# Optimization experiments

Hardware: AMD Instinct MI355X
Metric: run time of the kernel (lower is better)

## Reference

```python
import jax, jax.numpy as jnp
import numpy as np
from jax import lax

BLOCK_LEN = 128  # ctx_len 8192 / blocks 64
NEG_INF = -1e9


def setup_inputs() -> dict:
    key = jax.random.key(0)
    ks = jax.random.split(key, 8)
    N, L, Dm = 2, 8192, 4096
    W, H, dh = 1024, 16, 64  # width = d_model*0.25
    s = lambda fan: 1.0 / np.sqrt(fan)
    return {
        "inputs": jax.random.normal(ks[0], (N, L, Dm), jnp.float32),
        "conv_w": jax.random.normal(ks[1], (3, Dm, 3 * W), jnp.float32) * s(3 * Dm),
        "conv_b": jnp.zeros((3 * W,), jnp.float32),
        "wq": jax.random.normal(ks[2], (W, H, dh), jnp.float32) * s(W),
        "bq": jnp.zeros((H, dh), jnp.float32),
        "wk": jax.random.normal(ks[3], (W, H, dh), jnp.float32) * s(W),
        "bk": jnp.zeros((H, dh), jnp.float32),
        "wv": jax.random.normal(ks[4], (W, H, dh), jnp.float32) * s(W),
        "bv": jnp.zeros((H, dh), jnp.float32),
        "wo": jax.random.normal(ks[5], (H, dh, W), jnp.float32) * s(H * dh),
        "bo": jnp.zeros((W,), jnp.float32),
        "proj_w": jax.random.normal(ks[6], (W, Dm), jnp.float32) * s(W),
        "proj_b": jnp.zeros((Dm,), jnp.float32),
    }


def reference(inputs, conv_w, conv_b, wq, bq, wk, bk, wv, bv, wo, bo, proj_w, proj_b):
    N, L, Dm = inputs.shape
    # Conv1D(kernel=3, same padding) producing q,k,v concatenated
    x = lax.conv_general_dilated(
        inputs, conv_w, window_strides=(1,), padding="SAME",
        dimension_numbers=("NWC", "WIO", "NWC")) + conv_b
    q, k, v = jnp.split(x, 3, axis=-1)  # each [N, L, W]
    W_ = q.shape[-1]
    nb = L // BLOCK_LEN
    # row attention: independent causal attention within each block
    q = q.reshape(N * nb, BLOCK_LEN, W_)
    k = k.reshape(N * nb, BLOCK_LEN, W_)
    v = v.reshape(N * nb, BLOCK_LEN, W_)
    dh = wq.shape[-1]
    qh = jnp.einsum("btd,dhe->bthe", q, wq) + bq  # [B, T, H, dh]
    kh = jnp.einsum("btd,dhe->bthe", k, wk) + bk
    vh = jnp.einsum("btd,dhe->bthe", v, wv) + bv
    scale = 1.0 / jnp.sqrt(jnp.asarray(dh, qh.dtype))
    scores = jnp.einsum("bqhe,bkhe->bhqk", qh * scale, kh)
    causal = jnp.tril(jnp.ones((BLOCK_LEN, BLOCK_LEN), bool))
    scores = jnp.where(causal, scores, NEG_INF)
    p = jax.nn.softmax(scores, axis=-1)
    o = jnp.einsum("bhqk,bkhe->bqhe", p, vh)
    o = jnp.einsum("bqhe,hed->bqd", o, wo) + bo  # MHA output projection -> width
    o = o.reshape(N, L, W_)
    return o @ proj_w + proj_b  # final Dense(d_model)
```

## Files before the change

kernel.cpp:

```cpp
#include <hip/hip_runtime.h>
#include <hip/hip_bf16.h>
#include <stdint.h>

typedef __attribute__((ext_vector_type(8))) short short8;
typedef __attribute__((ext_vector_type(4))) float f32x4;

#define AS1 __attribute__((address_space(1)))
#define AS3 __attribute__((address_space(3)))

__device__ __forceinline__ short f2bf(float x) {
    __hip_bfloat16 h = __float2bfloat16(x);
    union { __hip_bfloat16 h; short s; } u; u.h = h; return u.s;
}

__device__ __forceinline__ void gload_lds16(const short* g, short* l) {
    __builtin_amdgcn_global_load_lds((const AS1 void*)g, (AS3 void*)l, 16, 0, 0);
}

#define BAR()        asm volatile("s_barrier" ::: "memory")
#define VMCNT_BAR(N) asm volatile("s_waitcnt vmcnt(" #N ")\n\ts_barrier" ::: "memory")

template<int TAPS, bool F32OUT>
__global__ __launch_bounds__(512, 2) void gemm256(
    const short* __restrict__ A, int lda,
    const short* __restrict__ BT, int ldb, long long tapB,
    void* __restrict__ Cout, int ldc,
    const float* __restrict__ bias, int Ktiles)
{
    __shared__ __align__(16) short As[2 * 2 * 256 * 32];
    __shared__ __align__(16) short Bs[2 * 2 * 256 * 32];
    const int tid = threadIdx.x, lane = tid & 63, wid = tid >> 6;
    const int wm = wid >> 2, wn = wid & 3;
    const int m0 = blockIdx.y * 256, n0 = blockIdx.x * 256;
    const size_t arow0 = (TAPS == 3) ? ((size_t)(m0 >> 13) * 8194 + (size_t)(m0 & 8191))
                                     : (size_t)m0;
    const size_t ldaS = (size_t)lda, ldbS = (size_t)ldb, tapBS = (size_t)tapB;
    const short* Abase0 = A + arow0 * ldaS;
    const short* Bbase0 = BT + (size_t)n0 * ldbS;
    const int c15 = lane & 15, g4 = (lane >> 4) * 4;
    const int swz = ((lane >> 4) ^ ((c15 >> 1) & 3)) * 8;
    const int srow = tid >> 2;
    const int schunk = (((tid & 3) ^ ((tid >> 3) & 3)) * 8);

#define STG_A(u, kh, buf) do { \
    const int tp_ = (TAPS == 3) ? ((u) >> 6) : 0; \
    const int kc_ = (TAPS == 3) ? (((u) & 63) << 6) : ((u) << 6); \
    const short* g_ = Abase0 + (size_t)tp_ * ldaS + kc_ + (kh) * 32 \
                      + (size_t)srow * ldaS + schunk; \
    short* l_ = As + (buf) * 16384 + (kh) * 8192 + wid * 512; \
    gload_lds16(g_, l_); \
    gload_lds16(g_ + 128 * ldaS, l_ + 4096); \
} while (0)

#define STG_B(u, kh, buf) do { \
    const int tp_ = (TAPS == 3) ? ((u) >> 6) : 0; \
    const int kc_ = (TAPS == 3) ? (((u) & 63) << 6) : ((u) << 6); \
    const short* g_ = Bbase0 + (size_t)tp_ * tapBS + kc_ + (kh) * 32 \
                      + (size_t)srow * ldbS + schunk; \
    short* l_ = Bs + (buf) * 16384 + (kh) * 8192 + wid * 512; \
    gload_lds16(g_, l_); \
    gload_lds16(g_ + 128 * ldbS, l_ + 4096); \
} while (0)

#define LDA_(buf, kk, mi) (*(const short8*)(As + (buf) * 16384 + (kk) * 8192 \
                           + (wm * 128 + (mi) * 16 + c15) * 32 + swz))
#define LDB_(buf, kk, nj) (*(const short8*)(Bs + (buf) * 16384 + (kk) * 8192 \
                           + (wn * 64 + (nj) * 16 + c15) * 32 + swz))

#define MFMA8x2(J0, J1) do { \
    __builtin_amdgcn_s_setprio(1); \
    _Pragma("unroll") \
    for (int mi_ = 0; mi_ < 8; ++mi_) \
        acc[mi_][J0] = __builtin_amdgcn_mfma_f32_16x16x32_bf16(af[mi_], b0, acc[mi_][J0], 0, 0, 0); \
    _Pragma("unroll") \
    for (int mi_ = 0; mi_ < 8; ++mi_) \
        acc[mi_][J1] = __builtin_amdgcn_mfma_f32_16x16x32_bf16(af[mi_], b1, acc[mi_][J1], 0, 0, 0); \
    __builtin_amdgcn_s_setprio(0); \
} while (0)

    f32x4 acc[8][4];
    #pragma unroll
    for (int i = 0; i < 8; ++i)
        #pragma unroll
        for (int j = 0; j < 4; ++j)
            acc[i][j] = (f32x4){0.f, 0.f, 0.f, 0.f};

    STG_A(0, 0, 0); STG_B(0, 0, 0); STG_A(0, 1, 0); STG_B(0, 1, 0);
    VMCNT_BAR(4);

    for (int t = 0; t < Ktiles; ++t) {
        const int c = t & 1, nb = c ^ 1;
        const bool st = (t + 1 < Ktiles);
        const int u = t + 1;
        short8 af[8], b0, b1;

        #pragma unroll
        for (int mi = 0; mi < 8; ++mi) af[mi] = LDA_(c, 0, mi);
        b0 = LDB_(c, 0, 0); b1 = LDB_(c, 0, 1);
        if (st) STG_A(u, 0, nb);
        BAR();
        MFMA8x2(0, 1);
        BAR();

        b0 = LDB_(c, 0, 2); b1 = LDB_(c, 0, 3);
        if (st) STG_B(u, 0, nb);
        if (st) { VMCNT_BAR(4); } else { VMCNT_BAR(0); }
        MFMA8x2(2, 3);
        BAR();

        #pragma unroll
        for (int mi = 0; mi < 8; ++mi) af[mi] = LDA_(c, 1, mi);
        b0 = LDB_(c, 1, 0); b1 = LDB_(c, 1, 1);
        if (st) STG_A(u, 1, nb);
        BAR();
        MFMA8x2(0, 1);
        BAR();

        b0 = LDB_(c, 1, 2); b1 = LDB_(c, 1, 3);
        if (st) STG_B(u, 1, nb);
        if (st) { VMCNT_BAR(4); } else { VMCNT_BAR(0); }
        MFMA8x2(2, 3);
        BAR();
    }

    float bv[4];
    #pragma unroll
    for (int nj = 0; nj < 4; ++nj)
        bv[nj] = bias ? bias[n0 + wn * 64 + nj * 16 + c15] : 0.f;
    #pragma unroll
    for (int mi = 0; mi < 8; ++mi) {
        #pragma unroll
        for (int r = 0; r < 4; ++r) {
            const size_t row = (size_t)m0 + wm * 128 + mi * 16 + g4 + r;
            #pragma unroll
            for (int nj = 0; nj < 4; ++nj) {
                const int col = n0 + wn * 64 + nj * 16 + c15;
                const float v = acc[mi][nj][r] + bv[nj];
                if (F32OUT) ((float*)Cout)[row * (size_t)ldc + col] = v;
                else        ((short*)Cout)[row * (size_t)ldc + col] = f2bf(v);
            }
        }
    }
#undef STG_A
#undef STG_B
#undef LDA_
#undef LDB_
#undef MFMA8x2
}

__global__ __launch_bounds__(256) void attn_kernel(
    const short* __restrict__ qh, const short* __restrict__ kh,
    const short* __restrict__ vh, short* __restrict__ obuf)
{
    __shared__ __align__(16) char smem[54272];
    short* qs = (short*)smem;
    short* ks = (short*)smem + 9216;
    short* vt = (short*)(smem + 36864);
    short* ps = (short*)smem;
    short* os = (short*)smem;

    const int tid = threadIdx.x, lane = tid & 63, wid = tid >> 6;
    const int h = blockIdx.x, b = blockIdx.y;
    const size_t base = (size_t)b * 128 * 1024 + (size_t)h * 64;

    for (int i = tid; i < 1024; i += 256) {
        const int row = i >> 3, c8 = i & 7;
        const size_t g = base + (size_t)row * 1024 + c8 * 8;
        *(short8*)(qs + row * 72 + c8 * 8) = *(const short8*)(qh + g);
        *(short8*)(ks + row * 72 + c8 * 8) = *(const short8*)(kh + g);
        short8 vv = *(const short8*)(vh + g);
        #pragma unroll
        for (int j = 0; j < 8; ++j) vt[(c8 * 8 + j) * 136 + row] = vv[j];
    }
    __syncthreads();

    const int c15 = lane & 15, g8 = (lane >> 4) * 8, g4 = (lane >> 4) * 4;
    const int r0 = wid * 32;

    f32x4 sacc[2][8];
    #pragma unroll
    for (int mi = 0; mi < 2; ++mi)
        #pragma unroll
        for (int nj = 0; nj < 8; ++nj)
            sacc[mi][nj] = (f32x4){0.f, 0.f, 0.f, 0.f};
    #pragma unroll
    for (int kk = 0; kk < 2; ++kk) {
        short8 aq[2];
        #pragma unroll
        for (int mi = 0; mi < 2; ++mi)
            aq[mi] = *(const short8*)(qs + (r0 + mi * 16 + c15) * 72 + kk * 32 + g8);
        #pragma unroll
        for (int nj = 0; nj < 8; ++nj) {
            short8 bk8 = *(const short8*)(ks + (nj * 16 + c15) * 72 + kk * 32 + g8);
            #pragma unroll
            for (int mi = 0; mi < 2; ++mi)
                sacc[mi][nj] = __builtin_amdgcn_mfma_f32_16x16x32_bf16(
                    aq[mi], bk8, sacc[mi][nj], 0, 0, 0);
        }
    }
    __syncthreads();

    #pragma unroll
    for (int mi = 0; mi < 2; ++mi) {
        #pragma unroll
        for (int r = 0; r < 4; ++r) {
            const int qrow = r0 + mi * 16 + g4 + r;
            float m = -3.0e38f, pv[8];
            #pragma unroll
            for (int nj = 0; nj < 8; ++nj) {
                float s = sacc[mi][nj][r] * 0.125f;
                if (nj * 16 + c15 > qrow) s = -1.0e9f;
                pv[nj] = s; m = fmaxf(m, s);
            }
            #pragma unroll
            for (int off = 8; off >= 1; off >>= 1) m = fmaxf(m, __shfl_xor(m, off));
            float sum = 0.f;
            #pragma unroll
            for (int nj = 0; nj < 8; ++nj) { float p = __expf(pv[nj] - m); pv[nj] = p; sum += p; }
            #pragma unroll
            for (int off = 8; off >= 1; off >>= 1) sum += __shfl_xor(sum, off);
            const float inv = 1.0f / sum;
            #pragma unroll
            for (int nj = 0; nj < 8; ++nj)
                ps[qrow * 136 + nj * 16 + c15] = f2bf(pv[nj] * inv);
        }
    }
    __syncthreads();

    f32x4 oacc[2][4];
    #pragma unroll
    for (int mi = 0; mi < 2; ++mi)
        #pragma unroll
        for (int nj = 0; nj < 4; ++nj)
            oacc[mi][nj] = (f32x4){0.f, 0.f, 0.f, 0.f};
    #pragma unroll
    for (int kt = 0; kt < 4; ++kt) {
        short8 ap[2];
        #pragma unroll
        for (int mi = 0; mi < 2; ++mi)
            ap[mi] = *(const short8*)(ps + (r0 + mi * 16 + c15) * 136 + kt * 32 + g8);
        #pragma unroll
        for (int nj = 0; nj < 4; ++nj) {
            short8 bv8 = *(const short8*)(vt + (nj * 16 + c15) * 136 + kt * 32 + g8);
            #pragma unroll
            for (int mi = 0; mi < 2; ++mi)
                oacc[mi][nj] = __builtin_amdgcn_mfma_f32_16x16x32_bf16(
                    ap[mi], bv8, oacc[mi][nj], 0, 0, 0);
        }
    }
    __syncthreads();

    #pragma unroll
    for (int mi = 0; mi < 2; ++mi)
        #pragma unroll
        for (int r = 0; r < 4; ++r)
            #pragma unroll
            for (int nj = 0; nj < 4; ++nj)
                os[(r0 + mi * 16 + g4 + r) * 72 + nj * 16 + c15] = f2bf(oacc[mi][nj][r]);
    __syncthreads();

    for (int i = tid; i < 1024; i += 256) {
        const int row = i >> 3, c8 = i & 7;
        *(short8*)(obuf + base + (size_t)row * 1024 + c8 * 8) =
            *(const short8*)(os + row * 72 + c8 * 8);
    }
}

__global__ void pad_convert_inputs(const float* __restrict__ in, short* __restrict__ out)
{
    const int row = blockIdx.x;
    const int n = row / 8194, l = row % 8194;
    short* orow = out + (size_t)row * 4096;
    if (l == 0 || l == 8193) {
        for (int i = threadIdx.x; i < 512; i += 256) {
            uint4 z; z.x = z.y = z.z = z.w = 0u;
            *(uint4*)(orow + i * 8) = z;
        }
    } else {
        const float* irow = in + ((size_t)n * 8192 + (l - 1)) * 4096;
        for (int i = threadIdx.x; i < 512; i += 256) {
            float4 a = *(const float4*)(irow + i * 8);
            float4 b = *(const float4*)(irow + i * 8 + 4);
            short8 v;
            v[0] = f2bf(a.x); v[1] = f2bf(a.y); v[2] = f2bf(a.z); v[3] = f2bf(a.w);
            v[4] = f2bf(b.x); v[5] = f2bf(b.y); v[6] = f2bf(b.z); v[7] = f2bf(b.w);
            *(short8*)(orow + i * 8) = v;
        }
    }
}

__global__ void transpose_convert(const float* __restrict__ in, short* __restrict__ out,
                                  int R, int C)
{
    __shared__ float tile[32][33];
    const int tx = threadIdx.x & 31, ty = threadIdx.x >> 5;
    const int bx = blockIdx.x * 32, by = blockIdx.y * 32;
    #pragma unroll
    for (int i = 0; i < 32; i += 8)
        tile[ty + i][tx] = in[(size_t)(by + ty + i) * C + bx + tx];
    __syncthreads();
    #pragma unroll
    for (int i = 0; i < 32; i += 8)
        out[(size_t)(bx + ty + i) * R + by + tx] = f2bf(tile[tx][ty + i]);
}

__global__ void convert_bf16(const float* __restrict__ in, short* __restrict__ out, int n8)
{
    const int idx = blockIdx.x * 256 + threadIdx.x;
    if (idx < n8) {
        float4 a = *(const float4*)(in + (size_t)idx * 8);
        float4 b = *(const float4*)(in + (size_t)idx * 8 + 4);
        short8 v;
        v[0] = f2bf(a.x); v[1] = f2bf(a.y); v[2] = f2bf(a.z); v[3] = f2bf(a.w);
        v[4] = f2bf(b.x); v[5] = f2bf(b.y); v[6] = f2bf(b.z); v[7] = f2bf(b.w);
        *(short8*)(out + (size_t)idx * 8) = v;
    }
}

__global__ void fuse_bias(const float* __restrict__ bo, const float* __restrict__ projw,
                          const float* __restrict__ projb, float* __restrict__ outb)
{
    const int j = blockIdx.x * 256 + threadIdx.x;
    float s = projb[j];
    for (int w = 0; w < 1024; ++w) s = fmaf(bo[w], projw[(size_t)w * 4096 + j], s);
    outb[j] = s;
}

extern "C" void kernel_launch(void* const* d_in, const int* in_sizes, int n_in,
                              void* d_out, int out_size, void* d_ws, size_t ws_size,
                              hipStream_t stream)
{
    const float* inputs = (const float*)d_in[0];
    const float* conv_w = (const float*)d_in[1];
    const float* conv_b = (const float*)d_in[2];
    const float* wq     = (const float*)d_in[3];
    const float* bq     = (const float*)d_in[4];
    const float* wk     = (const float*)d_in[5];
    const float* bk     = (const float*)d_in[6];
    const float* wv     = (const float*)d_in[7];
    const float* bv     = (const float*)d_in[8];
    const float* wo     = (const float*)d_in[9];
    const float* bo     = (const float*)d_in[10];
    const float* proj_w = (const float*)d_in[11];
    const float* proj_b = (const float*)d_in[12];

    char* ws = (char*)d_ws;
    short* in_pad = (short*)(ws + 0);
    short* w_bf   = (short*)(ws + 134283264);
    short* qkv    = (short*)(ws + 209780736);
    short* wq_t   = (short*)(ws + 310444032);
    short* wk_t   = (short*)(ws + 312541184);
    short* wv_t   = (short*)(ws + 314638336);
    short* wo_bf  = (short*)(ws + 316735488);
    short* proj_t = (short*)(ws + 318832640);
    short* WfT    = (short*)(ws + 327221248);
    float* bfused = (float*)(ws + 335609856);
    short* qh_buf = (short*)(ws + 0);
    short* kh_buf = (short*)(ws + 33554432);
    short* vh_buf = (short*)(ws + 67108864);
    short* o_buf  = (short*)(ws + 134283264);

    dim3 blk(256), blk5(512);

    pad_convert_inputs<<<16388, blk, 0, stream>>>(inputs, in_pad);
    for (int t = 0; t < 3; ++t)
        transpose_convert<<<dim3(96, 128), blk, 0, stream>>>(
            conv_w + (size_t)t * 4096 * 3072, w_bf + (size_t)t * 3072 * 4096, 4096, 3072);
    transpose_convert<<<dim3(32, 32), blk, 0, stream>>>(wq, wq_t, 1024, 1024);
    transpose_convert<<<dim3(32, 32), blk, 0, stream>>>(wk, wk_t, 1024, 1024);
    transpose_convert<<<dim3(32, 32), blk, 0, stream>>>(wv, wv_t, 1024, 1024);
    transpose_convert<<<dim3(128, 32), blk, 0, stream>>>(proj_w, proj_t, 1024, 4096);
    convert_bf16<<<512, blk, 0, stream>>>(wo, wo_bf, 131072);
    fuse_bias<<<16, blk, 0, stream>>>(bo, proj_w, proj_b, bfused);

    gemm256<1, false><<<dim3(4, 16), blk5, 0, stream>>>(
        proj_t, 1024, wo_bf, 1024, 0, WfT, 1024, nullptr, 16);
    gemm256<3, false><<<dim3(12, 64), blk5, 0, stream>>>(
        in_pad, 4096, w_bf, 4096, (long long)3072 * 4096, qkv, 3072, conv_b, 192);
    gemm256<1, false><<<dim3(4, 64), blk5, 0, stream>>>(
        qkv + 0,    3072, wq_t, 1024, 0, qh_buf, 1024, bq, 16);
    gemm256<1, false><<<dim3(4, 64), blk5, 0, stream>>>(
        qkv + 1024, 3072, wk_t, 1024, 0, kh_buf, 1024, bk, 16);
    gemm256<1, false><<<dim3(4, 64), blk5, 0, stream>>>(
        qkv + 2048, 3072, wv_t, 1024, 0, vh_buf, 1024, bv, 16);

    attn_kernel<<<dim3(16, 128), blk, 0, stream>>>(qh_buf, kh_buf, vh_buf, o_buf);

    gemm256<1, true><<<dim3(16, 64), blk5, 0, stream>>>(
        o_buf, 1024, WfT, 1024, 0, d_out, 4096, bfused, 16);
}
```

Before: 1.729 ms.

## Double-buffer GEMM LDS fragments in registers and prefetch across MFMA blocks

Restructures the gemm256 main loop so A/B fragments for the next MFMA block are loaded from LDS while the current 4x4 block of MFMAs runs. Fragments of the next tile are prefetched before the loop back. The MFMAs are regrouped into 4x4 sub-tiles and several barriers are dropped, with one lgkmcnt wait plus barrier at the end of each iteration. The aim is to hide LDS read latency behind matrix work and cut synchronisation, at the cost of more live vector registers and a possible spill risk under the 512x2 launch bound.

```diff
diff --git a/kernel.cpp b/kernel.cpp
--- a/kernel.cpp
+++ b/kernel.cpp
@@ -19,6 +19,7 @@
 
 #define BAR()        asm volatile("s_barrier" ::: "memory")
 #define VMCNT_BAR(N) asm volatile("s_waitcnt vmcnt(" #N ")\n\ts_barrier" ::: "memory")
+#define LGKM0_BAR()  asm volatile("s_waitcnt lgkmcnt(0)\n\ts_barrier" ::: "memory")
 
 template<int TAPS, bool F32OUT>
 __global__ __launch_bounds__(512, 2) void gemm256(
@@ -67,14 +68,15 @@
 #define LDB_(buf, kk, nj) (*(const short8*)(Bs + (buf) * 16384 + (kk) * 8192 \
                            + (wn * 64 + (nj) * 16 + c15) * 32 + swz))
 
-#define MFMA8x2(J0, J1) do { \
+#define MM(mi, nj, Av, Bv) acc[mi][nj] = \
+    __builtin_amdgcn_mfma_f32_16x16x32_bf16(Av, Bv, acc[mi][nj], 0, 0, 0)
+
+#define MFMA16(MB, A0, A1, A2, A3, B0, B1, B2, B3) do { \
     __builtin_amdgcn_s_setprio(1); \
-    _Pragma("unroll") \
-    for (int mi_ = 0; mi_ < 8; ++mi_) \
-        acc[mi_][J0] = __builtin_amdgcn_mfma_f32_16x16x32_bf16(af[mi_], b0, acc[mi_][J0], 0, 0, 0); \
-    _Pragma("unroll") \
-    for (int mi_ = 0; mi_ < 8; ++mi_) \
-        acc[mi_][J1] = __builtin_amdgcn_mfma_f32_16x16x32_bf16(af[mi_], b1, acc[mi_][J1], 0, 0, 0); \
+    MM((MB)+0, 0, A0, B0); MM((MB)+0, 1, A0, B1); MM((MB)+0, 2, A0, B2); MM((MB)+0, 3, A0, B3); \
+    MM((MB)+1, 0, A1, B0); MM((MB)+1, 1, A1, B1); MM((MB)+1, 2, A1, B2); MM((MB)+1, 3, A1, B3); \
+    MM((MB)+2, 0, A2, B0); MM((MB)+2, 1, A2, B1); MM((MB)+2, 2, A2, B2); MM((MB)+2, 3, A2, B3); \
+    MM((MB)+3, 0, A3, B0); MM((MB)+3, 1, A3, B1); MM((MB)+3, 2, A3, B2); MM((MB)+3, 3, A3, B3); \
     __builtin_amdgcn_s_setprio(0); \
 } while (0)
 
@@ -85,42 +87,47 @@
         for (int j = 0; j < 4; ++j)
             acc[i][j] = (f32x4){0.f, 0.f, 0.f, 0.f};
 
+    short8 afC0, afC1, afC2, afC3;
+    short8 afN0, afN1, afN2, afN3;
+    short8 bC0, bC1, bC2, bC3;
+    short8 bN0, bN1, bN2, bN3;
+
     STG_A(0, 0, 0); STG_B(0, 0, 0); STG_A(0, 1, 0); STG_B(0, 1, 0);
     VMCNT_BAR(4);
+    afC0 = LDA_(0, 0, 0); afC1 = LDA_(0, 0, 1); afC2 = LDA_(0, 0, 2); afC3 = LDA_(0, 0, 3);
+    bC0 = LDB_(0, 0, 0); bC1 = LDB_(0, 0, 1); bC2 = LDB_(0, 0, 2); bC3 = LDB_(0, 0, 3);
 
     for (int t = 0; t < Ktiles; ++t) {
         const int c = t & 1, nb = c ^ 1;
         const bool st = (t + 1 < Ktiles);
         const int u = t + 1;
-        short8 af[8], b0, b1;
-
-        #pragma unroll
-        for (int mi = 0; mi < 8; ++mi) af[mi] = LDA_(c, 0, mi);
-        b0 = LDB_(c, 0, 0); b1 = LDB_(c, 0, 1);
+
         if (st) STG_A(u, 0, nb);
         BAR();
-        MFMA8x2(0, 1);
-        BAR();
-
-        b0 = LDB_(c, 0, 2); b1 = LDB_(c, 0, 3);
+        afN0 = LDA_(c, 0, 4); afN1 = LDA_(c, 0, 5); afN2 = LDA_(c, 0, 6); afN3 = LDA_(c, 0, 7);
+        MFMA16(0, afC0, afC1, afC2, afC3, bC0, bC1, bC2, bC3);
+
         if (st) STG_B(u, 0, nb);
         if (st) { VMCNT_BAR(4); } else { VMCNT_BAR(0); }
-        MFMA8x2(2, 3);
-        BAR();
-
-        #pragma unroll
-        for (int mi = 0; mi < 8; ++mi) af[mi] = LDA_(c, 1, mi);
-        b0 = LDB_(c, 1, 0); b1 = LDB_(c, 1, 1);
+        afC0 = LDA_(c, 1, 0); afC1 = LDA_(c, 1, 1); afC2 = LDA_(c, 1, 2); afC3 = LDA_(c, 1, 3);
+        bN0 = LDB_(c, 1, 0); bN1 = LDB_(c, 1, 1); bN2 = LDB_(c, 1, 2); bN3 = LDB_(c, 1, 3);
+        MFMA16(4, afN0, afN1, afN2, afN3, bC0, bC1, bC2, bC3);
+
         if (st) STG_A(u, 1, nb);
         BAR();
-        MFMA8x2(0, 1);
-        BAR();
-
-        b0 = LDB_(c, 1, 2); b1 = LDB_(c, 1, 3);
+        afN0 = LDA_(c, 1, 4); afN1 = LDA_(c, 1, 5); afN2 = LDA_(c, 1, 6); afN3 = LDA_(c, 1, 7);
+        MFMA16(0, afC0, afC1, afC2, afC3, bN0, bN1, bN2, bN3);
+
         if (st) STG_B(u, 1, nb);
         if (st) { VMCNT_BAR(4); } else { VMCNT_BAR(0); }
-        MFMA8x2(2, 3);
-        BAR();
+        if (st) {
+            afC0 = LDA_(nb, 0, 0); afC1 = LDA_(nb, 0, 1);
+            afC2 = LDA_(nb, 0, 2); afC3 = LDA_(nb, 0, 3);
+            bC0 = LDB_(nb, 0, 0); bC1 = LDB_(nb, 0, 1);
+            bC2 = LDB_(nb, 0, 2); bC3 = LDB_(nb, 0, 3);
+        }
+        MFMA16(4, afN0, afN1, afN2, afN3, bN0, bN1, bN2, bN3);
+        LGKM0_BAR();
     }
 
     float bv[4];
@@ -145,7 +152,8 @@
 #undef STG_B
 #undef LDA_
 #undef LDB_
-#undef MFMA8x2
+#undef MM
+#undef MFMA16
 }
 
 __global__ __launch_bounds__(256) void attn_kernel(
```

New measurement: 1.841 ms. 6.5% more time.

## Deepen GEMM prefetch pipeline and batch Q/K/V projections into one launch

Applied to the files above, without the earlier changes.

The GEMM main loop is restructured to prefetch K-half tiles two steps ahead, using a finer-grained half-tile double buffer with adjusted vmcnt waits. The MFMA inner block becomes a 4x4 register tile, so fewer A fragments are held per phase. The three separate Q/K/V projection GEMMs are merged into a single 12x64-block launch, with a concatenated weight and bias and an interleaved qkvh output that the attention kernel reads with stride 3072. The aim is better latency hiding and fewer launches and tail effects, at the cost of more complex wait-count bookkeeping that must stay correct.

```diff
diff --git a/kernel.cpp b/kernel.cpp
--- a/kernel.cpp
+++ b/kernel.cpp
@@ -20,12 +20,12 @@
 #define BAR()        asm volatile("s_barrier" ::: "memory")
 #define VMCNT_BAR(N) asm volatile("s_waitcnt vmcnt(" #N ")\n\ts_barrier" ::: "memory")
 
-template<int TAPS, bool F32OUT>
+template<int TAPS, bool QKV, bool F32OUT>
 __global__ __launch_bounds__(512, 2) void gemm256(
     const short* __restrict__ A, int lda,
     const short* __restrict__ BT, int ldb, long long tapB,
     void* __restrict__ Cout, int ldc,
-    const float* __restrict__ bias, int Ktiles)
+    const float* __restrict__ bias, int KT)
 {
     __shared__ __align__(16) short As[2 * 2 * 256 * 32];
     __shared__ __align__(16) short Bs[2 * 2 * 256 * 32];
@@ -35,7 +35,7 @@
     const size_t arow0 = (TAPS == 3) ? ((size_t)(m0 >> 13) * 8194 + (size_t)(m0 & 8191))
                                      : (size_t)m0;
     const size_t ldaS = (size_t)lda, ldbS = (size_t)ldb, tapBS = (size_t)tapB;
-    const short* Abase0 = A + arow0 * ldaS;
+    const short* Abase0 = A + arow0 * ldaS + (QKV ? (n0 & ~1023) : 0);
     const short* Bbase0 = BT + (size_t)n0 * ldbS;
     const int c15 = lane & 15, g4 = (lane >> 4) * 4;
     const int swz = ((lane >> 4) ^ ((c15 >> 1) & 3)) * 8;
@@ -67,14 +67,15 @@
 #define LDB_(buf, kk, nj) (*(const short8*)(Bs + (buf) * 16384 + (kk) * 8192 \
                            + (wn * 64 + (nj) * 16 + c15) * 32 + swz))
 
-#define MFMA8x2(J0, J1) do { \
+#define MM(mi, nj, Av, Bv) acc[mi][nj] = \
+    __builtin_amdgcn_mfma_f32_16x16x32_bf16(Av, Bv, acc[mi][nj], 0, 0, 0)
+
+#define MFMA16(MB) do { \
     __builtin_amdgcn_s_setprio(1); \
-    _Pragma("unroll") \
-    for (int mi_ = 0; mi_ < 8; ++mi_) \
-        acc[mi_][J0] = __builtin_amdgcn_mfma_f32_16x16x32_bf16(af[mi_], b0, acc[mi_][J0], 0, 0, 0); \
-    _Pragma("unroll") \
-    for (int mi_ = 0; mi_ < 8; ++mi_) \
-        acc[mi_][J1] = __builtin_amdgcn_mfma_f32_16x16x32_bf16(af[mi_], b1, acc[mi_][J1], 0, 0, 0); \
+    MM((MB)+0, 0, a0, b0); MM((MB)+0, 1, a0, b1); MM((MB)+0, 2, a0, b2); MM((MB)+0, 3, a0, b3); \
+    MM((MB)+1, 0, a1, b0); MM((MB)+1, 1, a1, b1); MM((MB)+1, 2, a1, b2); MM((MB)+1, 3, a1, b3); \
+    MM((MB)+2, 0, a2, b0); MM((MB)+2, 1, a2, b1); MM((MB)+2, 2, a2, b2); MM((MB)+2, 3, a2, b3); \
+    MM((MB)+3, 0, a3, b0); MM((MB)+3, 1, a3, b1); MM((MB)+3, 2, a3, b2); MM((MB)+3, 3, a3, b3); \
     __builtin_amdgcn_s_setprio(0); \
 } while (0)
 
@@ -86,40 +87,40 @@
             acc[i][j] = (f32x4){0.f, 0.f, 0.f, 0.f};
 
     STG_A(0, 0, 0); STG_B(0, 0, 0); STG_A(0, 1, 0); STG_B(0, 1, 0);
-    VMCNT_BAR(4);
-
-    for (int t = 0; t < Ktiles; ++t) {
+    if (KT > 1) { STG_A(1, 0, 1); STG_B(1, 0, 1); VMCNT_BAR(8); }
+    else        { VMCNT_BAR(4); }
+
+    for (int t = 0; t < KT; ++t) {
         const int c = t & 1, nb = c ^ 1;
-        const bool st = (t + 1 < Ktiles);
-        const int u = t + 1;
-        short8 af[8], b0, b1;
-
-        #pragma unroll
-        for (int mi = 0; mi < 8; ++mi) af[mi] = LDA_(c, 0, mi);
-        b0 = LDB_(c, 0, 0); b1 = LDB_(c, 0, 1);
-        if (st) STG_A(u, 0, nb);
-        BAR();
-        MFMA8x2(0, 1);
-        BAR();
-
-        b0 = LDB_(c, 0, 2); b1 = LDB_(c, 0, 3);
-        if (st) STG_B(u, 0, nb);
-        if (st) { VMCNT_BAR(4); } else { VMCNT_BAR(0); }
-        MFMA8x2(2, 3);
-        BAR();
-
-        #pragma unroll
-        for (int mi = 0; mi < 8; ++mi) af[mi] = LDA_(c, 1, mi);
-        b0 = LDB_(c, 1, 0); b1 = LDB_(c, 1, 1);
-        if (st) STG_A(u, 1, nb);
-        BAR();
-        MFMA8x2(0, 1);
-        BAR();
-
-        b0 = LDB_(c, 1, 2); b1 = LDB_(c, 1, 3);
-        if (st) STG_B(u, 1, nb);
-        if (st) { VMCNT_BAR(4); } else { VMCNT_BAR(0); }
-        MFMA8x2(2, 3);
+        const bool st1 = (t + 1 < KT), st2 = (t + 2 < KT);
+        short8 a0, a1, a2, a3, b0, b1, b2, b3;
+
+        a0 = LDA_(c, 0, 0); a1 = LDA_(c, 0, 1); a2 = LDA_(c, 0, 2); a3 = LDA_(c, 0, 3);
+        b0 = LDB_(c, 0, 0); b1 = LDB_(c, 0, 1); b2 = LDB_(c, 0, 2); b3 = LDB_(c, 0, 3);
+        if (st1) STG_A(t + 1, 1, nb);
+        BAR();
+        MFMA16(0);
+        BAR();
+
+        a0 = LDA_(c, 0, 4); a1 = LDA_(c, 0, 5); a2 = LDA_(c, 0, 6); a3 = LDA_(c, 0, 7);
+        if (st1) STG_B(t + 1, 1, nb);
+        if (st1) { VMCNT_BAR(6); } else { VMCNT_BAR(0); }
+        MFMA16(4);
+        BAR();
+
+        a0 = LDA_(c, 1, 0); a1 = LDA_(c, 1, 1); a2 = LDA_(c, 1, 2); a3 = LDA_(c, 1, 3);
+        b0 = LDB_(c, 1, 0); b1 = LDB_(c, 1, 1); b2 = LDB_(c, 1, 2); b3 = LDB_(c, 1, 3);
+        if (st2) STG_A(t + 2, 0, c);
+        BAR();
+        MFMA16(0);
+        BAR();
+
+        a0 = LDA_(c, 1, 4); a1 = LDA_(c, 1, 5); a2 = LDA_(c, 1, 6); a3 = LDA_(c, 1, 7);
+        if (st2) STG_B(t + 2, 0, c);
+        if (st2)      { VMCNT_BAR(6); }
+        else if (st1) { VMCNT_BAR(4); }
+        else          { VMCNT_BAR(0); }
+        MFMA16(4);
         BAR();
     }
 
@@ -145,12 +146,12 @@
 #undef STG_B
 #undef LDA_
 #undef LDB_
-#undef MFMA8x2
+#undef MM
+#undef MFMA16
 }
 
 __global__ __launch_bounds__(256) void attn_kernel(
-    const short* __restrict__ qh, const short* __restrict__ kh,
-    const short* __restrict__ vh, short* __restrict__ obuf)
+    const short* __restrict__ qkvh, short* __restrict__ obuf)
 {
     __shared__ __align__(16) char smem[54272];
     short* qs = (short*)smem;
@@ -161,14 +162,14 @@
 
     const int tid = threadIdx.x, lane = tid & 63, wid = tid >> 6;
     const int h = blockIdx.x, b = blockIdx.y;
-    const size_t base = (size_t)b * 128 * 1024 + (size_t)h * 64;
+    const size_t base = (size_t)b * 128 * 3072 + (size_t)h * 64;
 
     for (int i = tid; i < 1024; i += 256) {
         const int row = i >> 3, c8 = i & 7;
-        const size_t g = base + (size_t)row * 1024 + c8 * 8;
-        *(short8*)(qs + row * 72 + c8 * 8) = *(const short8*)(qh + g);
-        *(short8*)(ks + row * 72 + c8 * 8) = *(const short8*)(kh + g);
-        short8 vv = *(const short8*)(vh + g);
+        const size_t g = base + (size_t)row * 3072 + c8 * 8;
+        *(short8*)(qs + row * 72 + c8 * 8) = *(const short8*)(qkvh + g);
+        *(short8*)(ks + row * 72 + c8 * 8) = *(const short8*)(qkvh + g + 1024);
+        short8 vv = *(const short8*)(qkvh + g + 2048);
         #pragma unroll
         for (int j = 0; j < 8; ++j) vt[(c8 * 8 + j) * 136 + row] = vv[j];
     }
@@ -261,7 +262,8 @@
 
     for (int i = tid; i < 1024; i += 256) {
         const int row = i >> 3, c8 = i & 7;
-        *(short8*)(obuf + base + (size_t)row * 1024 + c8 * 8) =
+        *(short8*)(obuf + (size_t)b * 128 * 1024 + (size_t)h * 64
+                   + (size_t)row * 1024 + c8 * 8) =
             *(const short8*)(os + row * 72 + c8 * 8);
     }
 }
@@ -324,6 +326,13 @@
     float s = projb[j];
     for (int w = 0; w < 1024; ++w) s = fmaf(bo[w], projw[(size_t)w * 4096 + j], s);
     outb[j] = s;
+}
+
+__global__ void concat_bias(const float* __restrict__ bq, const float* __restrict__ bk,
+                            const float* __restrict__ bv, float* __restrict__ outb)
+{
+    const int j = blockIdx.x * 256 + threadIdx.x;
+    outb[j] = (j < 1024) ? bq[j] : (j < 2048) ? bk[j - 1024] : bv[j - 2048];
 }
 
 extern "C" void kernel_launch(void* const* d_in, const int* in_sizes, int n_in,
@@ -349,15 +358,12 @@
     short* w_bf   = (short*)(ws + 134283264);
     short* qkv    = (short*)(ws + 209780736);
     short* wq_t   = (short*)(ws + 310444032);
-    short* wk_t   = (short*)(ws + 312541184);
-    short* wv_t   = (short*)(ws + 314638336);
     short* wo_bf  = (short*)(ws + 316735488);
     short* proj_t = (short*)(ws + 318832640);
     short* WfT    = (short*)(ws + 327221248);
     float* bfused = (float*)(ws + 335609856);
-    short* qh_buf = (short*)(ws + 0);
-    short* kh_buf = (short*)(ws + 33554432);
-    short* vh_buf = (short*)(ws + 67108864);
+    float* bqkv   = (float*)(ws + 335626240);
+    short* qkvh   = (short*)(ws + 0);
     short* o_buf  = (short*)(ws + 134283264);
 
     dim3 blk(256), blk5(512);
@@ -367,25 +373,22 @@
         transpose_convert<<<dim3(96, 128), blk, 0, stream>>>(
             conv_w + (size_t)t * 4096 * 3072, w_bf + (size_t)t * 3072 * 4096, 4096, 3072);
     transpose_convert<<<dim3(32, 32), blk, 0, stream>>>(wq, wq_t, 1024, 1024);
-    transpose_convert<<<dim3(32, 32), blk, 0, stream>>>(wk, wk_t, 1024, 1024);
-    transpose_convert<<<dim3(32, 32), blk, 0, stream>>>(wv, wv_t, 1024, 1024);
+    transpose_convert<<<dim3(32, 32), blk, 0, stream>>>(wk, wq_t + 1048576, 1024, 1024);
+    transpose_convert<<<dim3(32, 32), blk, 0, stream>>>(wv, wq_t + 2097152, 1024, 1024);
     transpose_convert<<<dim3(128, 32), blk, 0, stream>>>(proj_w, proj_t, 1024, 4096);
     convert_bf16<<<512, blk, 0, stream>>>(wo, wo_bf, 131072);
     fuse_bias<<<16, blk, 0, stream>>>(bo, proj_w, proj_b, bfused);
-
-    gemm256<1, false><<<dim3(4, 16), blk5, 0, stream>>>(
+    concat_bias<<<12, blk, 0, stream>>>(bq, bk, bv, bqkv);
+
+    gemm256<1, false, false><<<dim3(4, 16), blk5, 0, stream>>>(
         proj_t, 1024, wo_bf, 1024, 0, WfT, 1024, nullptr, 16);
-    gemm256<3, false><<<dim3(12, 64), blk5, 0, stream>>>(
+    gemm256<3, false, false><<<dim3(12, 64), blk5, 0, stream>>>(
         in_pad, 4096, w_bf, 4096, (long long)3072 * 4096, qkv, 3072, conv_b, 192);
-    gemm256<1, false><<<dim3(4, 64), blk5, 0, stream>>>(
-        qkv + 0,    3072, wq_t, 1024, 0, qh_buf, 1024, bq, 16);
-    gemm256<1, false><<<dim3(4, 64), blk5, 0, stream>>>(
-        qkv + 1024, 3072, wk_t, 1024, 0, kh_buf, 1024, bk, 16);
-    gemm256<1, false><<<dim3(4, 64), blk5, 0, stream>>>(
-        qkv + 2048, 3072, wv_t, 1024, 0, vh_buf, 1024, bv, 16);
-
-    attn_kernel<<<dim3(16, 128), blk, 0, stream>>>(qh_buf, kh_buf, vh_buf, o_buf);
-
-    gemm256<1, true><<<dim3(16, 64), blk5, 0, stream>>>(
+    gemm256<1, true, false><<<dim3(12, 64), blk5, 0, stream>>>(
+        qkv, 3072, wq_t, 1024, 0, qkvh, 3072, bqkv, 16);
+
+    attn_kernel<<<dim3(16, 128), blk, 0, stream>>>(qkvh, o_buf);
+
+    gemm256<1, false, true><<<dim3(16, 64), blk5, 0, stream>>>(
         o_buf, 1024, WfT, 1024, 0, d_out, 4096, bfused, 16);
 }
```

Result: no change. 1.715 ms (-0.8%).
